# Performance work log

Hardware: AMD Instinct MI355X
Metric: run time of the kernel (lower is better)

## Reference

```python
import jax, jax.numpy as jnp
import numpy as np


def _warp(x, flow):
    """Bilinear backward warp (grid_sample, zeros padding, pixel coords).
    x: [B,C,H,W], flow: [B,2,H,W] with flow[:,0]=dx, flow[:,1]=dy."""
    B, C, H, W = x.shape
    gx = jnp.arange(W, dtype=x.dtype)[None, None, :] + flow[:, 0]  # [B,H,W]
    gy = jnp.arange(H, dtype=x.dtype)[None, :, None] + flow[:, 1]  # [B,H,W]
    x0 = jnp.floor(gx)
    y0 = jnp.floor(gy)
    wx = gx - x0
    wy = gy - y0
    x0 = x0.astype(jnp.int32)
    y0 = y0.astype(jnp.int32)
    xf = x.reshape(B, C, H * W)

    def tap(yi, xi, w):
        valid = (xi >= 0) & (xi < W) & (yi >= 0) & (yi < H)
        idx = (jnp.clip(yi, 0, H - 1) * W + jnp.clip(xi, 0, W - 1)).reshape(B, 1, H * W)
        v = jnp.take_along_axis(xf, idx, axis=2).reshape(B, C, H, W)
        return v * (w * valid)[:, None]

    return (tap(y0, x0, (1 - wx) * (1 - wy))
            + tap(y0, x0 + 1, wx * (1 - wy))
            + tap(y0 + 1, x0, (1 - wx) * wy)
            + tap(y0 + 1, x0 + 1, wx * wy))


def _shift(flow, bias):
    # shift(Flow, motion): warp the flow field itself by a constant motion vector
    B, _, H, W = flow.shape
    const = jnp.broadcast_to(jnp.asarray(bias, flow.dtype).reshape(1, 2, 1, 1), (B, 2, H, W))
    return _warp(flow, const)


def _make_obmc(x, flow):
    vols = [_warp(x, flow)]
    for bias in ([0.0, 1.0], [1.0, 0.0], [0.0, -1.0], [-1.0, 0.0]):
        vols.append(_warp(x, _shift(flow, bias)))
    return jnp.concatenate(vols, axis=1)  # [B, 5*C, H, W]


def setup_inputs() -> dict:
    key = jax.random.key(0)
    k1, k2 = jax.random.split(key)
    x = jax.random.normal(k1, (4, 64, 256, 256), dtype=jnp.float32)
    flow = jax.random.normal(k2, (4, 2, 256, 256), dtype=jnp.float32) * 4.0
    return {"x": x, "flow": flow}


def reference(x, flow):
    return _make_obmc(x, flow)
```

## Files before the change

kernel.cpp:

```cpp
#include <hip/hip_runtime.h>
#include <hip/hip_fp16.h>

#define BB 4
#define CC 64
#define HH 256
#define WW 256
#define HWHW (HH * WW)

typedef float vf4 __attribute__((ext_vector_type(4)));

union H4 {
    __half2 h2[2];
    uint2 u;
};

__device__ __forceinline__ float4 ld4h(const __half* p) {
    const H4 r = *(const H4*)p;
    const float2 a = __half22float2(r.h2[0]);
    const float2 b = __half22float2(r.h2[1]);
    return make_float4(a.x, a.y, b.x, b.y);
}

__global__ __launch_bounds__(256) void transpose_xk(const float* __restrict__ x,
                                                    __half* __restrict__ xt) {
    __shared__ float tile[64][65];
    const int b = blockIdx.y;
    const int hw0 = blockIdx.x << 6;
    const int t = threadIdx.x;
    const float* xb = x + (size_t)b * CC * HWHW;

    const int cq = t >> 4;
    const int px4 = (t & 15) << 2;
#pragma unroll
    for (int k = 0; k < 4; ++k) {
        const int c = cq + (k << 4);
        const vf4 v = __builtin_nontemporal_load(
            (const vf4*)&xb[(size_t)c * HWHW + hw0 + px4]);
        tile[c][px4 + 0] = v.x;
        tile[c][px4 + 1] = v.y;
        tile[c][px4 + 2] = v.z;
        tile[c][px4 + 3] = v.w;
    }
    __syncthreads();
    __half* xtb = xt + ((size_t)b * HWHW << 6);
    const int hwq = t >> 4;
    const int c4 = (t & 15) << 2;
#pragma unroll
    for (int k = 0; k < 4; ++k) {
        const int hw = hwq + (k << 4);
        H4 h;
        h.h2[0] = __floats2half2_rn(tile[c4 + 0][hw], tile[c4 + 1][hw]);
        h.h2[1] = __floats2half2_rn(tile[c4 + 2][hw], tile[c4 + 3][hw]);
        *(uint2*)&xtb[((size_t)(hw0 + hw) << 6) + c4] = h.u;
    }
}

__global__ __launch_bounds__(256) void obmc_kernel(const __half* __restrict__ xt,
                                                   const float* __restrict__ flow,
                                                   float* __restrict__ out) {
    __shared__ int4 dOff[5][64];
    __shared__ float4 dW[5][64];
    __shared__ float sm[64][65];

    const int bid = ((blockIdx.x & 7) << 9) + (blockIdx.x >> 3);
    const int tx0 = (bid & 3) << 6;
    const int y = (bid >> 2) & 255;
    const int b = bid >> 10;
    const int t = threadIdx.x;
    const int wv = t >> 6;
    const int lane = t & 63;
    const int sp = lane >> 4;
    const int c4 = (lane & 15) << 2;

    const __half* xtb = xt + ((size_t)b * HWHW << 6);
    const float* fb = flow + (size_t)b * 2 * HWHW;
    float* ob = out + (size_t)b * 5 * CC * HWHW + (size_t)y * WW + tx0;

    const int oys[5] = {0, 1, 0, -1, 0};
    const int oxs[5] = {0, 0, 1, 0, -1};

    for (int idx = t; idx < 320; idx += 256) {
        const int g = idx >> 6, px = idx & 63;
        const int sy = y + oys[g];
        const int sx = tx0 + px + oxs[g];
        float fx = 0.f, fy = 0.f;
        if ((unsigned)sy < HH && (unsigned)sx < WW) {
            const int fo = sy * WW + sx;
            fx = fb[fo];
            fy = fb[HWHW + fo];
        }
        const float gx = (float)(tx0 + px) + fx;
        const float gy = (float)y + fy;
        const float x0f = floorf(gx);
        const float y0f = floorf(gy);
        const float fwx = gx - x0f;
        const float fwy = gy - y0f;
        const int ix0 = (int)x0f, iy0 = (int)y0f;
        const int ix1 = ix0 + 1, iy1 = iy0 + 1;
        const float vx0 = ((unsigned)ix0 < WW) ? 1.f : 0.f;
        const float vx1 = ((unsigned)ix1 < WW) ? 1.f : 0.f;
        const float vy0 = ((unsigned)iy0 < HH) ? 1.f : 0.f;
        const float vy1 = ((unsigned)iy1 < HH) ? 1.f : 0.f;
        const int xc0 = min(max(ix0, 0), WW - 1);
        const int xc1 = min(max(ix1, 0), WW - 1);
        const int yc0 = min(max(iy0, 0), HH - 1);
        const int yc1 = min(max(iy1, 0), HH - 1);
        dOff[g][px] = make_int4((yc0 * WW + xc0) << 6, (yc0 * WW + xc1) << 6,
                                (yc1 * WW + xc0) << 6, (yc1 * WW + xc1) << 6);
        dW[g][px] = make_float4((1.f - fwx) * (1.f - fwy) * vx0 * vy0,
                                fwx * (1.f - fwy) * vx1 * vy0,
                                (1.f - fwx) * fwy * vx0 * vy1,
                                fwx * fwy * vx1 * vy1);
    }
    __syncthreads();

    for (int g = 0; g < 5; ++g) {
        float4 acc[4];
#pragma unroll
        for (int i = 0; i < 4; ++i) {
            const int px = (wv << 4) + (i << 2) + sp;
            const int4 o = dOff[g][px];
            const float4 w = dW[g][px];
            const float4 v0 = ld4h(xtb + o.x + c4);
            const float4 v1 = ld4h(xtb + o.y + c4);
            const float4 v2 = ld4h(xtb + o.z + c4);
            const float4 v3 = ld4h(xtb + o.w + c4);
            float4 a;
            a.x = w.x * v0.x; a.y = w.x * v0.y; a.z = w.x * v0.z; a.w = w.x * v0.w;
            a.x = fmaf(w.y, v1.x, a.x); a.y = fmaf(w.y, v1.y, a.y);
            a.z = fmaf(w.y, v1.z, a.z); a.w = fmaf(w.y, v1.w, a.w);
            a.x = fmaf(w.z, v2.x, a.x); a.y = fmaf(w.z, v2.y, a.y);
            a.z = fmaf(w.z, v2.z, a.z); a.w = fmaf(w.z, v2.w, a.w);
            a.x = fmaf(w.w, v3.x, a.x); a.y = fmaf(w.w, v3.y, a.y);
            a.z = fmaf(w.w, v3.z, a.z); a.w = fmaf(w.w, v3.w, a.w);
            acc[i] = a;
        }
#pragma unroll
        for (int i = 0; i < 4; ++i) {
            const int px = (wv << 4) + (i << 2) + sp;
            sm[c4 + 0][px] = acc[i].x;
            sm[c4 + 1][px] = acc[i].y;
            sm[c4 + 2][px] = acc[i].z;
            sm[c4 + 3][px] = acc[i].w;
        }
        __syncthreads();
#pragma unroll
        for (int k = 0; k < 16; ++k) {
            const int c = (wv << 4) + k;
            __builtin_nontemporal_store(sm[c][lane],
                                        &ob[(size_t)(g * CC + c) * HWHW + lane]);
        }
        __syncthreads();
    }
}

extern "C" void kernel_launch(void* const* d_in, const int* in_sizes, int n_in,
                              void* d_out, int out_size, void* d_ws, size_t ws_size,
                              hipStream_t stream) {
    const float* x = (const float*)d_in[0];
    const float* flow = (const float*)d_in[1];
    float* out = (float*)d_out;
    __half* xt = (__half*)d_ws;

    transpose_xk<<<dim3(HWHW / 64, BB), 256, 0, stream>>>(x, xt);
    obmc_kernel<<<BB * HH * (WW / 64), 256, 0, stream>>>(xt, flow, out);
}
```

Before: 394.2 us.

## Double-buffer swizzled output tile, vectorize stores, pack tap offsets

Replaces the padded 64x65 shared staging tile with a double-buffered, XOR-swizzled 64x64 tile. This lets the write-out phase read float4 and issue 128-bit nontemporal stores instead of scalar stores, and removes the second barrier per group. Tap offsets are packed into int2 (base plus x/y deltas) to cut LDS footprint and reads. The swizzle must keep bank conflicts low for both the scalar writes and the vector reads. Dropping the trailing barrier depends on the two alternating buffers to avoid read/write races.

After: 395.0 us. No clear change (+0.2%).

```diff
diff --git a/kernel.cpp b/kernel.cpp
--- a/kernel.cpp
+++ b/kernel.cpp
@@ -19,6 +19,10 @@
     const float2 a = __half22float2(r.h2[0]);
     const float2 b = __half22float2(r.h2[1]);
     return make_float4(a.x, a.y, b.x, b.y);
+}
+
+__device__ __forceinline__ int smz(int k, int px) {
+    return px ^ (((k & 7) << 3) | ((k >> 3) << 2));
 }
 
 __global__ __launch_bounds__(256) void transpose_xk(const float* __restrict__ x,
@@ -58,9 +62,9 @@
 __global__ __launch_bounds__(256) void obmc_kernel(const __half* __restrict__ xt,
                                                    const float* __restrict__ flow,
                                                    float* __restrict__ out) {
-    __shared__ int4 dOff[5][64];
+    __shared__ int2 dOffp[5][64];
     __shared__ float4 dW[5][64];
-    __shared__ float sm[64][65];
+    __shared__ float sm[2][64][64];
 
     const int bid = ((blockIdx.x & 7) << 9) + (blockIdx.x >> 3);
     const int tx0 = (bid & 3) << 6;
@@ -70,7 +74,8 @@
     const int wv = t >> 6;
     const int lane = t & 63;
     const int sp = lane >> 4;
-    const int c4 = (lane & 15) << 2;
+    const int kk = lane & 15;
+    const int c4 = kk << 2;
 
     const __half* xtb = xt + ((size_t)b * HWHW << 6);
     const float* fb = flow + (size_t)b * 2 * HWHW;
@@ -105,8 +110,10 @@
         const int xc1 = min(max(ix1, 0), WW - 1);
         const int yc0 = min(max(iy0, 0), HH - 1);
         const int yc1 = min(max(iy1, 0), HH - 1);
-        dOff[g][px] = make_int4((yc0 * WW + xc0) << 6, (yc0 * WW + xc1) << 6,
-                                (yc1 * WW + xc0) << 6, (yc1 * WW + xc1) << 6);
+        const int base = ((yc0 * WW + xc0) << 6);
+        const int dx = (xc1 - xc0) << 6;
+        const int dyv = (yc1 - yc0) << 14;
+        dOffp[g][px] = make_int2(base, (dyv << 16) | dx);
         dW[g][px] = make_float4((1.f - fwx) * (1.f - fwy) * vx0 * vy0,
                                 fwx * (1.f - fwy) * vx1 * vy0,
                                 (1.f - fwx) * fwy * vx0 * vy1,
@@ -115,16 +122,20 @@
     __syncthreads();
 
     for (int g = 0; g < 5; ++g) {
+        const int p = g & 1;
         float4 acc[4];
 #pragma unroll
         for (int i = 0; i < 4; ++i) {
             const int px = (wv << 4) + (i << 2) + sp;
-            const int4 o = dOff[g][px];
+            const int2 o = dOffp[g][px];
             const float4 w = dW[g][px];
-            const float4 v0 = ld4h(xtb + o.x + c4);
-            const float4 v1 = ld4h(xtb + o.y + c4);
-            const float4 v2 = ld4h(xtb + o.z + c4);
-            const float4 v3 = ld4h(xtb + o.w + c4);
+            const int o0 = o.x + c4;
+            const int dx = o.y & 0xffff;
+            const int dyv = ((unsigned)o.y) >> 16;
+            const float4 v0 = ld4h(xtb + o0);
+            const float4 v1 = ld4h(xtb + o0 + dx);
+            const float4 v2 = ld4h(xtb + o0 + dyv);
+            const float4 v3 = ld4h(xtb + o0 + dyv + dx);
             float4 a;
             a.x = w.x * v0.x; a.y = w.x * v0.y; a.z = w.x * v0.z; a.w = w.x * v0.w;
             a.x = fmaf(w.y, v1.x, a.x); a.y = fmaf(w.y, v1.y, a.y);
@@ -138,19 +149,21 @@
 #pragma unroll
         for (int i = 0; i < 4; ++i) {
             const int px = (wv << 4) + (i << 2) + sp;
-            sm[c4 + 0][px] = acc[i].x;
-            sm[c4 + 1][px] = acc[i].y;
-            sm[c4 + 2][px] = acc[i].z;
-            sm[c4 + 3][px] = acc[i].w;
+            const int zp = smz(kk, px);
+            sm[p][c4 + 0][zp] = acc[i].x;
+            sm[p][c4 + 1][zp] = acc[i].y;
+            sm[p][c4 + 2][zp] = acc[i].z;
+            sm[p][c4 + 3][zp] = acc[i].w;
         }
         __syncthreads();
 #pragma unroll
-        for (int k = 0; k < 16; ++k) {
-            const int c = (wv << 4) + k;
-            __builtin_nontemporal_store(sm[c][lane],
-                                        &ob[(size_t)(g * CC + c) * HWHW + lane]);
+        for (int m = 0; m < 4; ++m) {
+            const int c = (wv << 4) + (m << 2) + sp;
+            const int px4 = kk << 2;
+            const vf4 v = *(const vf4*)&sm[p][c][smz(c >> 2, px4)];
+            __builtin_nontemporal_store(
+                v, (vf4*)&ob[(size_t)(g * CC + c) * HWHW + px4]);
         }
-        __syncthreads();
     }
 }
 
```
